# Kernel tuning notes

Hardware: AMD Instinct MI355X
Metric: run time of the kernel (lower is better)

Reference implementation:

```python
import jax, jax.numpy as jnp
import numpy as np

D_MODEL = 2048
NUM_HEADS = 16
D_K = D_MODEL // NUM_HEADS
THETA = 10000.0
BATCH, SEQ = 2, 2048


def setup_inputs() -> dict:
    key = jax.random.key(0)
    ks = jax.random.split(key, 5)
    scale = 1.0 / np.sqrt(D_MODEL)
    x = jax.random.normal(ks[0], (BATCH, SEQ, D_MODEL), dtype=jnp.float32)
    token_positions = jnp.broadcast_to(jnp.arange(SEQ, dtype=jnp.int32)[None, :], (BATCH, SEQ))
    Wq = jax.random.normal(ks[1], (D_MODEL, D_MODEL), dtype=jnp.float32) * scale
    Wk = jax.random.normal(ks[2], (D_MODEL, D_MODEL), dtype=jnp.float32) * scale
    Wv = jax.random.normal(ks[3], (D_MODEL, D_MODEL), dtype=jnp.float32) * scale
    Wo = jax.random.normal(ks[4], (D_MODEL, D_MODEL), dtype=jnp.float32) * scale
    return {"x": x, "token_positions": token_positions, "Wq": Wq, "Wk": Wk, "Wv": Wv, "Wo": Wo}


def _apply_rope(t, positions):
    # t: [b, h, s, d_k]; positions: [b, s]. Interleaved-pair rotation.
    half = D_K // 2
    inv_freq = THETA ** (-jnp.arange(0, half, dtype=jnp.float32) * 2.0 / D_K)  # [half]
    ang = positions.astype(jnp.float32)[:, :, None] * inv_freq[None, None, :]  # [b, s, half]
    cos = jnp.cos(ang)[:, None, :, :]  # [b, 1, s, half]
    sin = jnp.sin(ang)[:, None, :, :]
    t2 = t.reshape(*t.shape[:-1], half, 2)
    x1, x2 = t2[..., 0], t2[..., 1]
    r1 = x1 * cos - x2 * sin
    r2 = x1 * sin + x2 * cos
    return jnp.stack([r1, r2], axis=-1).reshape(t.shape)


def reference(x, token_positions, Wq, Wk, Wv, Wo):
    b, s, _ = x.shape
    # Linear layers compute x @ W^T (weight stored as [out, in], no bias)
    def proj(w):
        y = jnp.einsum('bsd,ed->bse', x, w)
        return y.reshape(b, s, NUM_HEADS, D_K).transpose(0, 2, 1, 3)  # b h s d
    Q, K, V = proj(Wq), proj(Wk), proj(Wv)
    Q = _apply_rope(Q, token_positions)
    K = _apply_rope(K, token_positions)
    scores = jnp.einsum('bhqd,bhkd->bhqk', Q, K) / jnp.sqrt(jnp.float32(D_K))
    causal = jnp.tril(jnp.ones((s, s), dtype=bool))
    scores = jnp.where(causal[None, None], scores, jnp.finfo(scores.dtype).min)
    attn = jax.nn.softmax(scores, axis=-1)
    out = jnp.einsum('bhqk,bhkd->bhqd', attn, V)  # b h s d
    out = out.transpose(0, 2, 1, 3).reshape(b, s, D_MODEL)
    return jnp.einsum('bse,de->bsd', out, Wo)
```

## Files before the change

kernel.cpp:

```cpp
#include <hip/hip_runtime.h>
#include <cstdint>
#include <cstddef>

#define D_MODEL 2048
#define NHEAD 16
#define DK 128
#define SEQ 2048
#define BATCH 2
#define NTOK (BATCH * SEQ)
#define NQB 32

typedef __bf16 bf16;
typedef __bf16 bf16x2 __attribute__((ext_vector_type(2)));
typedef __bf16 bf16x4 __attribute__((ext_vector_type(4)));
typedef __bf16 bf16x8 __attribute__((ext_vector_type(8)));
typedef float f32x4 __attribute__((ext_vector_type(4)));

__device__ __forceinline__ void g2lds16(const void* g, void* l) {
  __builtin_amdgcn_global_load_lds(
      (const __attribute__((address_space(1))) void*)g,
      (__attribute__((address_space(3))) void*)l, 16, 0, 0);
}

__device__ __forceinline__ void cstore(float* p, float v) { *p = v; }
__device__ __forceinline__ void cstore(bf16* p, float v) { *p = (bf16)v; }

#define BAR()                              \
  {                                        \
    asm volatile("" ::: "memory");         \
    __builtin_amdgcn_s_barrier();          \
    asm volatile("" ::: "memory");         \
  }

__global__ void k_f32_to_bf16(const float* __restrict__ in, bf16* __restrict__ out, int n4) {
  int i = blockIdx.x * blockDim.x + threadIdx.x;
  if (i >= n4) return;
  const float4 v = ((const float4*)in)[i];
  bf16x4 o = {(bf16)v.x, (bf16)v.y, (bf16)v.z, (bf16)v.w};
  ((bf16x4*)out)[i] = o;
}

__global__ void k_w4_to_bf16(const float* __restrict__ W0, const float* __restrict__ W1,
                             const float* __restrict__ W2, const float* __restrict__ W3,
                             bf16* __restrict__ o0, bf16* __restrict__ o1,
                             bf16* __restrict__ o2, bf16* __restrict__ o3, int n4) {
  const float* in;
  bf16* out;
  switch (blockIdx.y) {
    case 0: in = W0; out = o0; break;
    case 1: in = W1; out = o1; break;
    case 2: in = W2; out = o2; break;
    default: in = W3; out = o3;
  }
  int i = blockIdx.x * blockDim.x + threadIdx.x;
  if (i >= n4) return;
  const float4 v = ((const float4*)in)[i];
  bf16x4 o = {(bf16)v.x, (bf16)v.y, (bf16)v.z, (bf16)v.w};
  ((bf16x4*)out)[i] = o;
}

__global__ void k_rope(bf16* __restrict__ Q, bf16* __restrict__ K, const int* __restrict__ pos) {
  int id = blockIdx.x * 256 + threadIdx.x;
  bf16* T = blockIdx.y ? K : Q;
  int f = id & 63;
  int h = (id >> 6) & 15;
  int row = id >> 10;
  float p = (float)pos[row];
  float ang = p * exp2f((float)f * -0.20762050593121503f);
  float s, c;
  __sincosf(ang, &s, &c);
  size_t base = (size_t)row * D_MODEL + h * DK + 2 * f;
  bf16x2 v = *(bf16x2*)&T[base];
  float x1 = (float)v[0], x2 = (float)v[1];
  bf16x2 o = {(bf16)(x1 * c - x2 * s), (bf16)(x1 * s + x2 * c)};
  *(bf16x2*)&T[base] = o;
}

__global__ __launch_bounds__(512, 1) void k_gemm8(
    const bf16* __restrict__ A, const bf16* __restrict__ B0p, const bf16* __restrict__ B1p,
    const bf16* __restrict__ B2p, bf16* __restrict__ C0, bf16* __restrict__ C1,
    bf16* __restrict__ C2, int M, int N, int K) {
  const bf16* Bp = B0p;
  bf16* Cp = C0;
  if (blockIdx.z == 1) { Bp = B1p; Cp = C1; }
  else if (blockIdx.z == 2) { Bp = B2p; Cp = C2; }

  __shared__ bf16 Ab[2][256 * 64];
  __shared__ bf16 Bb[2][256 * 64];

  const int t = threadIdx.x;
  const int wid = t >> 6, lane = t & 63;
  const int wr = wid >> 2, wc = wid & 3;
  const int lr = lane & 15, lg = lane >> 4;
  const int bm = blockIdx.y, bn = blockIdx.x;
  const size_t arow0 = (size_t)bm * 256;
  const size_t brow0 = (size_t)bn * 256;

  const int srow = wid * 8 + (lane >> 3);
  const int schunk = ((lane & 7) ^ ((lane >> 3) & 7)) * 8;

#define STG(X, row0, k0, lb, h)                                                \
  {                                                                            \
    g2lds16(&(X)[((row0) + (h)*128 + srow) * (size_t)K + (k0) + schunk],       \
            &(lb)[((h)*128 + wid * 8) * 64]);                                  \
    g2lds16(&(X)[((row0) + (h)*128 + 64 + srow) * (size_t)K + (k0) + schunk],  \
            &(lb)[((h)*128 + 64 + wid * 8) * 64]);                             \
  }
#define LDA8(lb, mh, m, kk) \
  (*(const bf16x8*)&(lb)[((mh)*128 + wr * 64 + (m)*16 + lr) * 64 + ((((kk)*4 + lg) ^ (lr & 7)) * 8)])
#define LDB8(lb, nh, n, kk) \
  (*(const bf16x8*)&(lb)[((nh)*128 + wc * 32 + (n)*16 + lr) * 64 + ((((kk)*4 + lg) ^ (lr & 7)) * 8)])

  const int T = K >> 6;

  STG(A, arow0, 0, Ab[0], 0);
  STG(A, arow0, 0, Ab[0], 1);
  STG(Bp, brow0, 0, Bb[0], 0);
  STG(Bp, brow0, 0, Bb[0], 1);
  STG(A, arow0, 64, Ab[1], 0);

  f32x4 acc[2][2][4][2] = {};

  for (int tt = 0; tt < T; ++tt) {
    const int cur = tt & 1;
    const bf16* Ac = Ab[cur];
    const bf16* Bc = Bb[cur];
    bf16* Aw = Ab[cur];
    bf16* An = Ab[cur ^ 1];
    bf16* Bn = Bb[cur ^ 1];
    const int k1 = (tt + 1) << 6;
    const int k2 = (tt + 2) << 6;
    const bool pf1 = (tt + 1 < T);
    const bool pf2 = (tt + 2 < T);

    if (tt == T - 1) {
      asm volatile("s_waitcnt vmcnt(0)" ::: "memory");
    } else {
      asm volatile("s_waitcnt vmcnt(2)" ::: "memory");
    }
    BAR();

    bf16x8 a[4][2], b[2][2];

#pragma unroll
    for (int m = 0; m < 4; ++m)
#pragma unroll
      for (int kk = 0; kk < 2; ++kk) a[m][kk] = LDA8(Ac, 0, m, kk);
#pragma unroll
    for (int n = 0; n < 2; ++n)
#pragma unroll
      for (int kk = 0; kk < 2; ++kk) b[n][kk] = LDB8(Bc, 0, n, kk);
    if (pf1) {
      STG(A, arow0, k1, An, 1);
      STG(Bp, brow0, k1, Bn, 0);
    }
    __builtin_amdgcn_s_setprio(1);
#pragma unroll
    for (int m = 0; m < 4; ++m)
#pragma unroll
      for (int n = 0; n < 2; ++n)
#pragma unroll
        for (int kk = 0; kk < 2; ++kk)
          acc[0][0][m][n] =
              __builtin_amdgcn_mfma_f32_16x16x32_bf16(a[m][kk], b[n][kk], acc[0][0][m][n], 0, 0, 0);
    __builtin_amdgcn_s_setprio(0);
    BAR();

#pragma unroll
    for (int n = 0; n < 2; ++n)
#pragma unroll
      for (int kk = 0; kk < 2; ++kk) b[n][kk] = LDB8(Bc, 1, n, kk);
    if (pf1) STG(Bp, brow0, k1, Bn, 1);
    __builtin_amdgcn_s_setprio(1);
#pragma unroll
    for (int m = 0; m < 4; ++m)
#pragma unroll
      for (int n = 0; n < 2; ++n)
#pragma unroll
        for (int kk = 0; kk < 2; ++kk)
          acc[0][1][m][n] =
              __builtin_amdgcn_mfma_f32_16x16x32_bf16(a[m][kk], b[n][kk], acc[0][1][m][n], 0, 0, 0);
    __builtin_amdgcn_s_setprio(0);
    BAR();

#pragma unroll
    for (int m = 0; m < 4; ++m)
#pragma unroll
      for (int kk = 0; kk < 2; ++kk) a[m][kk] = LDA8(Ac, 1, m, kk);
    if (pf2) STG(A, arow0, k2, Aw, 0);
    __builtin_amdgcn_s_setprio(1);
#pragma unroll
    for (int m = 0; m < 4; ++m)
#pragma unroll
      for (int n = 0; n < 2; ++n)
#pragma unroll
        for (int kk = 0; kk < 2; ++kk)
          acc[1][1][m][n] =
              __builtin_amdgcn_mfma_f32_16x16x32_bf16(a[m][kk], b[n][kk], acc[1][1][m][n], 0, 0, 0);
    __builtin_amdgcn_s_setprio(0);
    BAR();

#pragma unroll
    for (int n = 0; n < 2; ++n)
#pragma unroll
      for (int kk = 0; kk < 2; ++kk) b[n][kk] = LDB8(Bc, 0, n, kk);
    __builtin_amdgcn_s_setprio(1);
#pragma unroll
    for (int m = 0; m < 4; ++m)
#pragma unroll
      for (int n = 0; n < 2; ++n)
#pragma unroll
        for (int kk = 0; kk < 2; ++kk)
          acc[1][0][m][n] =
              __builtin_amdgcn_mfma_f32_16x16x32_bf16(a[m][kk], b[n][kk], acc[1][0][m][n], 0, 0, 0);
    __builtin_amdgcn_s_setprio(0);
  }

#pragma unroll
  for (int mh = 0; mh < 2; ++mh)
#pragma unroll
    for (int nh = 0; nh < 2; ++nh)
#pragma unroll
      for (int m = 0; m < 4; ++m) {
        size_t rowb = arow0 + mh * 128 + wr * 64 + m * 16 + lg * 4;
#pragma unroll
        for (int n = 0; n < 2; ++n) {
          size_t col = brow0 + nh * 128 + wc * 32 + n * 16 + lr;
#pragma unroll
          for (int r = 0; r < 4; ++r) Cp[(rowb + r) * N + col] = (bf16)acc[mh][nh][m][n][r];
        }
      }
#undef STG
#undef LDA8
#undef LDB8
}

template <typename OutT>
__global__ __launch_bounds__(256, 2) void k_gemm_nt(
    const bf16* __restrict__ A, const bf16* __restrict__ B0, const bf16* __restrict__ B1,
    const bf16* __restrict__ B2, OutT* __restrict__ C0, OutT* __restrict__ C1,
    OutT* __restrict__ C2, int M, int N, int K) {
  const bf16* Bp = B0;
  OutT* Cp = C0;
  if (blockIdx.z == 1) { Bp = B1; Cp = C1; }
  else if (blockIdx.z == 2) { Bp = B2; Cp = C2; }

  __shared__ bf16 As[128 * 32];
  __shared__ bf16 Bs[128 * 32];

  const int t = threadIdx.x;
  const int w = t >> 6;
  const int lane = t & 63;
  const int lr = lane & 15;
  const int lg = lane >> 4;
  const int wr = w >> 1, wc = w & 1;
  const int bm = blockIdx.y, bn = blockIdx.x;

  f32x4 acc[4][4] = {};

  const int srow = lane >> 2;
  const int scol = (lane & 3) * 8;

  const int kt_iters = K >> 5;
  for (int kt = 0; kt < kt_iters; ++kt) {
    const int kbase = kt * 32;
#pragma unroll
    for (int i = 0; i < 2; ++i) {
      int chunk = w * 2 + i;
      int row = chunk * 16 + srow;
      g2lds16(&A[(size_t)(bm * 128 + row) * K + kbase + scol], &As[chunk * 512]);
      g2lds16(&Bp[(size_t)(bn * 128 + row) * K + kbase + scol], &Bs[chunk * 512]);
    }
    asm volatile("s_waitcnt vmcnt(0)" ::: "memory");
    __syncthreads();

    bf16x8 af[4], bfr[4];
#pragma unroll
    for (int m = 0; m < 4; ++m)
      af[m] = *(const bf16x8*)&As[(wr * 64 + m * 16 + lr) * 32 + lg * 8];
#pragma unroll
    for (int n = 0; n < 4; ++n)
      bfr[n] = *(const bf16x8*)&Bs[(wc * 64 + n * 16 + lr) * 32 + lg * 8];
#pragma unroll
    for (int m = 0; m < 4; ++m)
#pragma unroll
      for (int n = 0; n < 4; ++n)
        acc[m][n] = __builtin_amdgcn_mfma_f32_16x16x32_bf16(af[m], bfr[n], acc[m][n], 0, 0, 0);
    __syncthreads();
  }

#pragma unroll
  for (int m = 0; m < 4; ++m) {
    int rowb = bm * 128 + wr * 64 + m * 16 + lg * 4;
#pragma unroll
    for (int n = 0; n < 4; ++n) {
      int col = bn * 128 + wc * 64 + n * 16 + lr;
#pragma unroll
      for (int r = 0; r < 4; ++r) cstore(&Cp[(size_t)(rowb + r) * N + col], acc[m][n][r]);
    }
  }
}

__global__ __launch_bounds__(256, 2) void k_attn(const bf16* __restrict__ Q,
                                                 const bf16* __restrict__ K,
                                                 const bf16* __restrict__ V,
                                                 bf16* __restrict__ O) {
  const int wg = blockIdx.x;
  const int g = wg & 7;
  const int i = wg >> 3;
  const int bh = g + 8 * (i & 3);
  const int pr = i >> 2;
  const int b = bh >> 4, h = bh & 15;

  const int t = threadIdx.x;
  const int w = t >> 6, lane = t & 63;
  const int lr = lane & 15, lg = lane >> 4;

  const size_t rowbase = (size_t)b * SEQ;
  const int hoff = h * DK;

  __shared__ bf16 Ks[2][64 * 128];
  __shared__ uint32_t VTu[2][128 * 32];
  __shared__ bf16 Pb[4][16 * 64];

  const int kp = t & 31;
  const int d0s = (t >> 5) * 16;

  const float scale = 0.08838834764831845f;
  const float FIXM = 8.0f;

  bf16x8 sa0, sa1, sb0, sb1;
  int cur = 0;

  const int krow_l = lane >> 4;
  const int kchunk = lane & 15;

  for (int qsel = 0; qsel < 2; ++qsel) {
    const int qblk = qsel ? pr : (NQB - 1 - pr);
    const int qb = qblk * 64;
    const int ktiles = qblk + 1;

    bf16x8 qf[4];
    {
      size_t qrow = rowbase + qb + w * 16 + lr;
#pragma unroll
      for (int c = 0; c < 4; ++c)
        qf[c] = *(const bf16x8*)&Q[qrow * D_MODEL + hoff + c * 32 + lg * 8];
    }

    f32x4 o[8] = {};
    f32x4 lrow = {};

#pragma unroll
    for (int j = 0; j < 4; ++j) {
      int row = w * 16 + j * 4 + krow_l;
      int chunk = kchunk ^ (j * 4 + krow_l);
      g2lds16(&K[(rowbase + row) * D_MODEL + hoff + chunk * 8],
              &Ks[cur][(size_t)(w * 16 + j * 4) * 128]);
    }
    {
      const bf16* vp0 = &V[(rowbase + 2 * kp) * D_MODEL + hoff + d0s];
      sa0 = *(const bf16x8*)vp0;
      sa1 = *(const bf16x8*)(vp0 + 8);
      sb0 = *(const bf16x8*)(vp0 + D_MODEL);
      sb1 = *(const bf16x8*)(vp0 + D_MODEL + 8);
    }

    for (int kt = 0; kt < ktiles; ++kt) {
      const int k0 = kt * 64;
#pragma unroll
      for (int j = 0; j < 8; ++j) {
        int d = d0s + j;
        bf16x2 p0 = {sa0[j], sb0[j]};
        VTu[cur][d * 32 + (kp ^ ((d & 7) << 2))] = *(const uint32_t*)&p0;
      }
#pragma unroll
      for (int j = 0; j < 8; ++j) {
        int d = d0s + 8 + j;
        bf16x2 p1 = {sa1[j], sb1[j]};
        VTu[cur][d * 32 + (kp ^ ((d & 7) << 2))] = *(const uint32_t*)&p1;
      }
      asm volatile("s_waitcnt vmcnt(0)" ::: "memory");
      __syncthreads();

      if (kt + 1 < ktiles) {
#pragma unroll
        for (int j = 0; j < 4; ++j) {
          int row = w * 16 + j * 4 + krow_l;
          int chunk = kchunk ^ (j * 4 + krow_l);
          g2lds16(&K[(rowbase + k0 + 64 + row) * D_MODEL + hoff + chunk * 8],
                  &Ks[cur ^ 1][(size_t)(w * 16 + j * 4) * 128]);
        }
        const bf16* vp0 = &V[(rowbase + k0 + 64 + 2 * kp) * D_MODEL + hoff + d0s];
        sa0 = *(const bf16x8*)vp0;
        sa1 = *(const bf16x8*)(vp0 + 8);
        sb0 = *(const bf16x8*)(vp0 + D_MODEL);
        sb1 = *(const bf16x8*)(vp0 + D_MODEL + 8);
      }

      f32x4 sc[4];
      __builtin_amdgcn_s_setprio(1);
#pragma unroll
      for (int tt = 0; tt < 4; ++tt) {
        f32x4 a = {};
#pragma unroll
        for (int c = 0; c < 4; ++c) {
          bf16x8 kf = *(const bf16x8*)&Ks[cur][(tt * 16 + lr) * 128 + (((c * 4 + lg) ^ lr) * 8)];
          a = __builtin_amdgcn_mfma_f32_16x16x32_bf16(qf[c], kf, a, 0, 0, 0);
        }
        sc[tt] = a * scale;
      }
      __builtin_amdgcn_s_setprio(0);

      const int qrow0 = qb + w * 16 + lg * 4;
      if (k0 + 64 > qb + w * 16) {
#pragma unroll
        for (int tt = 0; tt < 4; ++tt) {
          int kcol = k0 + tt * 16 + lr;
#pragma unroll
          for (int r = 0; r < 4; ++r)
            if (kcol > qrow0 + r) sc[tt][r] = -3.0e38f;
        }
      }

#pragma unroll
      for (int tt = 0; tt < 4; ++tt)
#pragma unroll
        for (int r = 0; r < 4; ++r) {
          float p = __expf(sc[tt][r] - FIXM);
          sc[tt][r] = p;
          lrow[r] += p;
        }

#pragma unroll
      for (int tt = 0; tt < 4; ++tt)
#pragma unroll
        for (int r = 0; r < 4; ++r) {
          int q = lg * 4 + r;
          int col = tt * 16 + lr;
          Pb[w][q * 64 + (col ^ ((q & 7) << 3))] = (bf16)sc[tt][r];
        }
      asm volatile("s_waitcnt lgkmcnt(0)" ::: "memory");
      bf16x8 pf0 = *(const bf16x8*)&Pb[w][lr * 64 + ((lg * 8) ^ ((lr & 7) << 3))];
      bf16x8 pf1 = *(const bf16x8*)&Pb[w][lr * 64 + ((32 + lg * 8) ^ ((lr & 7) << 3))];

      __builtin_amdgcn_s_setprio(1);
#pragma unroll
      for (int nt = 0; nt < 8; ++nt) {
        int d = nt * 16 + lr;
        bf16x8 vf0 = *(const bf16x8*)&VTu[cur][d * 32 + ((lg * 4) ^ ((d & 7) << 2))];
        bf16x8 vf1 = *(const bf16x8*)&VTu[cur][d * 32 + ((16 + lg * 4) ^ ((d & 7) << 2))];
        o[nt] = __builtin_amdgcn_mfma_f32_16x16x32_bf16(pf0, vf0, o[nt], 0, 0, 0);
        o[nt] = __builtin_amdgcn_mfma_f32_16x16x32_bf16(pf1, vf1, o[nt], 0, 0, 0);
      }
      __builtin_amdgcn_s_setprio(0);
      cur ^= 1;
    }

#pragma unroll
    for (int off = 8; off >= 1; off >>= 1)
#pragma unroll
      for (int r = 0; r < 4; ++r) lrow[r] += __shfl_xor(lrow[r], off);

    size_t orow = rowbase + qb + w * 16 + lg * 4;
#pragma unroll
    for (int nt = 0; nt < 8; ++nt)
#pragma unroll
      for (int r = 0; r < 4; ++r)
        O[(orow + r) * D_MODEL + hoff + nt * 16 + lr] = (bf16)(o[nt][r] / lrow[r]);
  }
}

extern "C" void kernel_launch(void* const* d_in, const int* in_sizes, int n_in, void* d_out,
                              int out_size, void* d_ws, size_t ws_size, hipStream_t stream) {
  const float* x = (const float*)d_in[0];
  const int* pos = (const int*)d_in[1];
  const float* Wq = (const float*)d_in[2];
  const float* Wk = (const float*)d_in[3];
  const float* Wv = (const float*)d_in[4];
  const float* Wo = (const float*)d_in[5];
  float* out = (float*)d_out;

  char* ws = (char*)d_ws;
  const size_t MB = 1u << 20;
  bf16* xb  = (bf16*)(ws);
  bf16* wqb = (bf16*)(ws + 16 * MB);
  bf16* wkb = (bf16*)(ws + 24 * MB);
  bf16* wvb = (bf16*)(ws + 32 * MB);
  bf16* wob = (bf16*)(ws + 40 * MB);
  bf16* Qb  = (bf16*)(ws + 48 * MB);
  bf16* Kb  = (bf16*)(ws + 64 * MB);
  bf16* Vb  = (bf16*)(ws + 80 * MB);
  bf16* AOb = (bf16*)(ws + 96 * MB);

  {
    int n4 = NTOK * D_MODEL / 4;
    k_f32_to_bf16<<<(n4 + 255) / 256, 256, 0, stream>>>(x, xb, n4);
    int w4 = D_MODEL * D_MODEL / 4;
    k_w4_to_bf16<<<dim3((w4 + 255) / 256, 4), 256, 0, stream>>>(
        Wq, Wk, Wv, Wo, wqb, wkb, wvb, wob, w4);
  }
  {
    dim3 g(D_MODEL / 256, NTOK / 256, 3);
    k_gemm8<<<g, 512, 0, stream>>>(xb, wqb, wkb, wvb, Qb, Kb, Vb, NTOK, D_MODEL, D_MODEL);
  }
  {
    int pairs = NTOK * NHEAD * 64;
    k_rope<<<dim3(pairs / 256, 2), 256, 0, stream>>>(Qb, Kb, pos);
  }
  k_attn<<<dim3(NQB * NHEAD * BATCH / 2, 1, 1), 256, 0, stream>>>(Qb, Kb, Vb, AOb);
  {
    dim3 g(D_MODEL / 128, NTOK / 128, 1);
    k_gemm_nt<float><<<g, 256, 0, stream>>>(AOb, wob, wob, wob, out, out, out, NTOK, D_MODEL, D_MODEL);
  }
}
```

Baseline: 273.9 us.

## Use 128x256 pipelined GEMM for QKV and output projections with grouped block mapping

```diff
diff --git a/kernel.cpp b/kernel.cpp
--- a/kernel.cpp
+++ b/kernel.cpp
@@ -76,50 +76,59 @@
   *(bf16x2*)&T[base] = o;
 }
 
-__global__ __launch_bounds__(512, 1) void k_gemm8(
+template <typename OutT>
+__global__ __launch_bounds__(512, 1) void k_gemmP(
     const bf16* __restrict__ A, const bf16* __restrict__ B0p, const bf16* __restrict__ B1p,
-    const bf16* __restrict__ B2p, bf16* __restrict__ C0, bf16* __restrict__ C1,
-    bf16* __restrict__ C2, int M, int N, int K) {
+    const bf16* __restrict__ B2p, OutT* __restrict__ C0, OutT* __restrict__ C1,
+    OutT* __restrict__ C2, int M, int N, int K) {
+  const int wg = blockIdx.x;
+  const int g = wg & 7;
+  const int i = wg >> 3;
+  const int z = i >> 5;
+  const int bm = i & 31;
+  const int bn = g;
+
   const bf16* Bp = B0p;
-  bf16* Cp = C0;
-  if (blockIdx.z == 1) { Bp = B1p; Cp = C1; }
-  else if (blockIdx.z == 2) { Bp = B2p; Cp = C2; }
-
-  __shared__ bf16 Ab[2][256 * 64];
+  OutT* Cp = C0;
+  if (z == 1) { Bp = B1p; Cp = C1; }
+  else if (z == 2) { Bp = B2p; Cp = C2; }
+
+  __shared__ bf16 Ab[2][128 * 64];
   __shared__ bf16 Bb[2][256 * 64];
 
   const int t = threadIdx.x;
   const int wid = t >> 6, lane = t & 63;
   const int wr = wid >> 2, wc = wid & 3;
   const int lr = lane & 15, lg = lane >> 4;
-  const int bm = blockIdx.y, bn = blockIdx.x;
-  const size_t arow0 = (size_t)bm * 256;
+  const size_t arow0 = (size_t)bm * 128;
   const size_t brow0 = (size_t)bn * 256;
 
   const int srow = wid * 8 + (lane >> 3);
   const int schunk = ((lane & 7) ^ ((lane >> 3) & 7)) * 8;
 
-#define STG(X, row0, k0, lb, h)                                                \
-  {                                                                            \
-    g2lds16(&(X)[((row0) + (h)*128 + srow) * (size_t)K + (k0) + schunk],       \
-            &(lb)[((h)*128 + wid * 8) * 64]);                                  \
-    g2lds16(&(X)[((row0) + (h)*128 + 64 + srow) * (size_t)K + (k0) + schunk],  \
-            &(lb)[((h)*128 + 64 + wid * 8) * 64]);                             \
+#define STGA(X, k0, lb, h) \
+  g2lds16(&(X)[(arow0 + (h)*64 + srow) * (size_t)K + (k0) + schunk], &(lb)[((h)*64 + wid * 8) * 64]);
+#define STGB(X, k0, lb, h)                                                        \
+  {                                                                               \
+    g2lds16(&(X)[(brow0 + (h)*128 + srow) * (size_t)K + (k0) + schunk],           \
+            &(lb)[((h)*128 + wid * 8) * 64]);                                     \
+    g2lds16(&(X)[(brow0 + (h)*128 + 64 + srow) * (size_t)K + (k0) + schunk],      \
+            &(lb)[((h)*128 + 64 + wid * 8) * 64]);                                \
   }
 #define LDA8(lb, mh, m, kk) \
-  (*(const bf16x8*)&(lb)[((mh)*128 + wr * 64 + (m)*16 + lr) * 64 + ((((kk)*4 + lg) ^ (lr & 7)) * 8)])
+  (*(const bf16x8*)&(lb)[((mh)*64 + wr * 32 + (m)*16 + lr) * 64 + ((((kk)*4 + lg) ^ (lr & 7)) * 8)])
 #define LDB8(lb, nh, n, kk) \
   (*(const bf16x8*)&(lb)[((nh)*128 + wc * 32 + (n)*16 + lr) * 64 + ((((kk)*4 + lg) ^ (lr & 7)) * 8)])
 
   const int T = K >> 6;
 
-  STG(A, arow0, 0, Ab[0], 0);
-  STG(A, arow0, 0, Ab[0], 1);
-  STG(Bp, brow0, 0, Bb[0], 0);
-  STG(Bp, brow0, 0, Bb[0], 1);
-  STG(A, arow0, 64, Ab[1], 0);
-
-  f32x4 acc[2][2][4][2] = {};
+  STGA(A, 0, Ab[0], 0);
+  STGA(A, 0, Ab[0], 1);
+  STGB(Bp, 0, Bb[0], 0);
+  STGB(Bp, 0, Bb[0], 1);
+  STGA(A, 64, Ab[1], 0);
+
+  f32x4 acc[2][2][2][2] = {};
 
   for (int tt = 0; tt < T; ++tt) {
     const int cur = tt & 1;
@@ -136,14 +145,14 @@
     if (tt == T - 1) {
       asm volatile("s_waitcnt vmcnt(0)" ::: "memory");
     } else {
-      asm volatile("s_waitcnt vmcnt(2)" ::: "memory");
+      asm volatile("s_waitcnt vmcnt(1)" ::: "memory");
     }
     BAR();
 
-    bf16x8 a[4][2], b[2][2];
-
-#pragma unroll
-    for (int m = 0; m < 4; ++m)
+    bf16x8 a[2][2], b[2][2];
+
+#pragma unroll
+    for (int m = 0; m < 2; ++m)
 #pragma unroll
       for (int kk = 0; kk < 2; ++kk) a[m][kk] = LDA8(Ac, 0, m, kk);
 #pragma unroll
@@ -151,12 +160,12 @@
 #pragma unroll
       for (int kk = 0; kk < 2; ++kk) b[n][kk] = LDB8(Bc, 0, n, kk);
     if (pf1) {
-      STG(A, arow0, k1, An, 1);
-      STG(Bp, brow0, k1, Bn, 0);
+      STGA(A, k1, An, 1);
+      STGB(Bp, k1, Bn, 0);
     }
     __builtin_amdgcn_s_setprio(1);
 #pragma unroll
-    for (int m = 0; m < 4; ++m)
+    for (int m = 0; m < 2; ++m)
 #pragma unroll
       for (int n = 0; n < 2; ++n)
 #pragma unroll
@@ -170,10 +179,10 @@
     for (int n = 0; n < 2; ++n)
 #pragma unroll
       for (int kk = 0; kk < 2; ++kk) b[n][kk] = LDB8(Bc, 1, n, kk);
-    if (pf1) STG(Bp, brow0, k1, Bn, 1);
+    if (pf1) STGB(Bp, k1, Bn, 1);
     __builtin_amdgcn_s_setprio(1);
 #pragma unroll
-    for (int m = 0; m < 4; ++m)
+    for (int m = 0; m < 2; ++m)
 #pragma unroll
       for (int n = 0; n < 2; ++n)
 #pragma unroll
@@ -184,13 +193,13 @@
     BAR();
 
 #pragma unroll
-    for (int m = 0; m < 4; ++m)
+    for (int m = 0; m < 2; ++m)
 #pragma unroll
       for (int kk = 0; kk < 2; ++kk) a[m][kk] = LDA8(Ac, 1, m, kk);
-    if (pf2) STG(A, arow0, k2, Aw, 0);
+    if (pf2) STGA(A, k2, Aw, 0);
     __builtin_amdgcn_s_setprio(1);
 #pragma unroll
-    for (int m = 0; m < 4; ++m)
+    for (int m = 0; m < 2; ++m)
 #pragma unroll
       for (int n = 0; n < 2; ++n)
 #pragma unroll
@@ -206,7 +215,7 @@
       for (int kk = 0; kk < 2; ++kk) b[n][kk] = LDB8(Bc, 0, n, kk);
     __builtin_amdgcn_s_setprio(1);
 #pragma unroll
-    for (int m = 0; m < 4; ++m)
+    for (int m = 0; m < 2; ++m)
 #pragma unroll
       for (int n = 0; n < 2; ++n)
 #pragma unroll
@@ -221,84 +230,19 @@
 #pragma unroll
     for (int nh = 0; nh < 2; ++nh)
 #pragma unroll
-      for (int m = 0; m < 4; ++m) {
-        size_t rowb = arow0 + mh * 128 + wr * 64 + m * 16 + lg * 4;
+      for (int m = 0; m < 2; ++m) {
+        size_t rowb = arow0 + mh * 64 + wr * 32 + m * 16 + lg * 4;
 #pragma unroll
         for (int n = 0; n < 2; ++n) {
           size_t col = brow0 + nh * 128 + wc * 32 + n * 16 + lr;
 #pragma unroll
-          for (int r = 0; r < 4; ++r) Cp[(rowb + r) * N + col] = (bf16)acc[mh][nh][m][n][r];
-        }
-      }
-#undef STG
+          for (int r = 0; r < 4; ++r) cstore(&Cp[(rowb + r) * N + col], acc[mh][nh][m][n][r]);
+        }
+      }
+#undef STGA
+#undef STGB
 #undef LDA8
 #undef LDB8
-}
-
-template <typename OutT>
-__global__ __launch_bounds__(256, 2) void k_gemm_nt(
-    const bf16* __restrict__ A, const bf16* __restrict__ B0, const bf16* __restrict__ B1,
-    const bf16* __restrict__ B2, OutT* __restrict__ C0, OutT* __restrict__ C1,
-    OutT* __restrict__ C2, int M, int N, int K) {
-  const bf16* Bp = B0;
-  OutT* Cp = C0;
-  if (blockIdx.z == 1) { Bp = B1; Cp = C1; }
-  else if (blockIdx.z == 2) { Bp = B2; Cp = C2; }
-
-  __shared__ bf16 As[128 * 32];
-  __shared__ bf16 Bs[128 * 32];
-
-  const int t = threadIdx.x;
-  const int w = t >> 6;
-  const int lane = t & 63;
-  const int lr = lane & 15;
-  const int lg = lane >> 4;
-  const int wr = w >> 1, wc = w & 1;
-  const int bm = blockIdx.y, bn = blockIdx.x;
-
-  f32x4 acc[4][4] = {};
-
-  const int srow = lane >> 2;
-  const int scol = (lane & 3) * 8;
-
-  const int kt_iters = K >> 5;
-  for (int kt = 0; kt < kt_iters; ++kt) {
-    const int kbase = kt * 32;
-#pragma unroll
-    for (int i = 0; i < 2; ++i) {
-      int chunk = w * 2 + i;
-      int row = chunk * 16 + srow;
-      g2lds16(&A[(size_t)(bm * 128 + row) * K + kbase + scol], &As[chunk * 512]);
-      g2lds16(&Bp[(size_t)(bn * 128 + row) * K + kbase + scol], &Bs[chunk * 512]);
-    }
-    asm volatile("s_waitcnt vmcnt(0)" ::: "memory");
-    __syncthreads();
-
-    bf16x8 af[4], bfr[4];
-#pragma unroll
-    for (int m = 0; m < 4; ++m)
-      af[m] = *(const bf16x8*)&As[(wr * 64 + m * 16 + lr) * 32 + lg * 8];
-#pragma unroll
-    for (int n = 0; n < 4; ++n)
-      bfr[n] = *(const bf16x8*)&Bs[(wc * 64 + n * 16 + lr) * 32 + lg * 8];
-#pragma unroll
-    for (int m = 0; m < 4; ++m)
-#pragma unroll
-      for (int n = 0; n < 4; ++n)
-        acc[m][n] = __builtin_amdgcn_mfma_f32_16x16x32_bf16(af[m], bfr[n], acc[m][n], 0, 0, 0);
-    __syncthreads();
-  }
-
-#pragma unroll
-  for (int m = 0; m < 4; ++m) {
-    int rowb = bm * 128 + wr * 64 + m * 16 + lg * 4;
-#pragma unroll
-    for (int n = 0; n < 4; ++n) {
-      int col = bn * 128 + wc * 64 + n * 16 + lr;
-#pragma unroll
-      for (int r = 0; r < 4; ++r) cstore(&Cp[(size_t)(rowb + r) * N + col], acc[m][n][r]);
-    }
-  }
 }
 
 __global__ __launch_bounds__(256, 2) void k_attn(const bf16* __restrict__ Q,
@@ -500,17 +444,13 @@
     k_w4_to_bf16<<<dim3((w4 + 255) / 256, 4), 256, 0, stream>>>(
         Wq, Wk, Wv, Wo, wqb, wkb, wvb, wob, w4);
   }
-  {
-    dim3 g(D_MODEL / 256, NTOK / 256, 3);
-    k_gemm8<<<g, 512, 0, stream>>>(xb, wqb, wkb, wvb, Qb, Kb, Vb, NTOK, D_MODEL, D_MODEL);
-  }
+  k_gemmP<bf16><<<768, 512, 0, stream>>>(xb, wqb, wkb, wvb, Qb, Kb, Vb,
+                                         NTOK, D_MODEL, D_MODEL);
   {
     int pairs = NTOK * NHEAD * 64;
     k_rope<<<dim3(pairs / 256, 2), 256, 0, stream>>>(Qb, Kb, pos);
   }
   k_attn<<<dim3(NQB * NHEAD * BATCH / 2, 1, 1), 256, 0, stream>>>(Qb, Kb, Vb, AOb);
-  {
-    dim3 g(D_MODEL / 128, NTOK / 128, 1);
-    k_gemm_nt<float><<<g, 256, 0, stream>>>(AOb, wob, wob, wob, out, out, out, NTOK, D_MODEL, D_MODEL);
-  }
-}
+  k_gemmP<float><<<256, 512, 0, stream>>>(AOb, wob, wob, wob, out, out, out,
+                                          NTOK, D_MODEL, D_MODEL);
+}
```

New measurement: 288.7 us. 5.4% more time.
